# Performance work log

Hardware: AMD Instinct MI355X
Metric: run time of the kernel (lower is better)

Reference implementation:

```python
import jax, jax.numpy as jnp
import numpy as np

B, W, WIN_IN = 8, 2048, 1024
D, NH, DFF, L, KS = 512, 8, 2048, 4, 4
NGENES, G = 20000, 2048


def _ln(x, g, b, eps=1e-5):
    m = jnp.mean(x, -1, keepdims=True)
    v = jnp.var(x, -1, keepdims=True)
    return (x - m) * jax.lax.rsqrt(v + eps) * g + b


def _mha(q_in, kv_in, qkv_w, qkv_b, out_w, out_b, nh):
    d = q_in.shape[-1]
    hd = d // nh
    wq, wk, wv = qkv_w[:d], qkv_w[d:2 * d], qkv_w[2 * d:]
    bq, bk, bv = qkv_b[:d], qkv_b[d:2 * d], qkv_b[2 * d:]
    q = (q_in @ wq.T + bq).reshape(q_in.shape[0], q_in.shape[1], nh, hd)
    k = (kv_in @ wk.T + bk).reshape(kv_in.shape[0], kv_in.shape[1], nh, hd)
    v = (kv_in @ wv.T + bv).reshape(kv_in.shape[0], kv_in.shape[1], nh, hd)
    scores = jnp.einsum('bqhd,bkhd->bhqk', q, k) / jnp.sqrt(jnp.asarray(hd, q.dtype))
    a = jax.nn.softmax(scores, axis=-1)
    o = jnp.einsum('bhqk,bkhd->bqhd', a, v).reshape(q_in.shape[0], q_in.shape[1], d)
    return o @ out_w.T + out_b


def _posenc(S, d, dtype):
    pos = jnp.arange(S, dtype=jnp.float32)[:, None]
    div = jnp.exp(jnp.arange(0, d, 2, dtype=jnp.float32) * (-np.log(10000.0) / d))
    pe = jnp.zeros((S, d), jnp.float32)
    pe = pe.at[:, 0::2].set(jnp.sin(pos * div)).at[:, 1::2].set(jnp.cos(pos * div))
    return pe.astype(dtype)


def setup_inputs():
    key = jax.random.key(0)
    ks_ = jax.random.split(key, 12)

    def n(k, shape, s=0.02):
        return jax.random.normal(k, shape, jnp.float32) * s

    return dict(
        windows=jax.random.normal(ks_[0], (B, W, WIN_IN), jnp.float32),
        gene_ids=jax.random.randint(ks_[1], (G,), 0, NGENES),
        W_window=n(ks_[2], (D, WIN_IN)),
        enc_qkv_w=n(ks_[3], (L, 3 * D, D)),
        enc_qkv_b=jnp.zeros((L, 3 * D), jnp.float32),
        enc_out_w=n(ks_[4], (L, D, D)),
        enc_out_b=jnp.zeros((L, D), jnp.float32),
        enc_ln1_g=jnp.ones((L, D), jnp.float32),
        enc_ln1_b=jnp.zeros((L, D), jnp.float32),
        enc_ln2_g=jnp.ones((L, D), jnp.float32),
        enc_ln2_b=jnp.zeros((L, D), jnp.float32),
        enc_ff1_w=n(ks_[5], (L, DFF, D)),
        enc_ff1_b=jnp.zeros((L, DFF), jnp.float32),
        enc_ff2_w=n(ks_[6], (L, D, DFF)),
        enc_ff2_b=jnp.zeros((L, D), jnp.float32),
        gene_embed=n(ks_[7], (NGENES, D), 1.0),
        ca_qkv_w=n(ks_[8], (3 * D, D)),
        ca_qkv_b=jnp.zeros((3 * D,), jnp.float32),
        ca_out_w=n(ks_[9], (D, D)),
        ca_out_b=jnp.zeros((D,), jnp.float32),
        ro_ln_g=jnp.ones((D,), jnp.float32),
        ro_ln_b=jnp.zeros((D,), jnp.float32),
        ro_w=n(ks_[10], (1, D)),
        ro_b=jnp.zeros((1,), jnp.float32),
    )


def reference(windows, gene_ids, W_window, enc_qkv_w, enc_qkv_b, enc_out_w,
              enc_out_b, enc_ln1_g, enc_ln1_b, enc_ln2_g, enc_ln2_b,
              enc_ff1_w, enc_ff1_b, enc_ff2_w, enc_ff2_b, gene_embed,
              ca_qkv_w, ca_qkv_b, ca_out_w, ca_out_b, ro_ln_g, ro_ln_b,
              ro_w, ro_b):
    # proj_window (Linear, no bias; dropout inactive in eval)
    x = windows @ W_window.T                          # [B, W, D]
    Bn, Wn, _ = x.shape
    # AvgPool1d(kernel=stride=KS) along the window axis
    x = x.reshape(Bn, Wn // KS, KS, D).mean(axis=2)   # [B, S, D]
    S = x.shape[1]
    x = x + _posenc(S, D, x.dtype)[None]
    # pre-LN TransformerEncoder, relu FFN, no final norm
    for i in range(L):
        h = _ln(x, enc_ln1_g[i], enc_ln1_b[i])
        x = x + _mha(h, h, enc_qkv_w[i], enc_qkv_b[i], enc_out_w[i], enc_out_b[i], NH)
        h = _ln(x, enc_ln2_g[i], enc_ln2_b[i])
        x = x + (jax.nn.relu(h @ enc_ff1_w[i].T + enc_ff1_b[i]) @ enc_ff2_w[i].T + enc_ff2_b[i])
    # gene queries -> cross attention over encoded windows
    q = jnp.broadcast_to(gene_embed[gene_ids][None], (Bn, gene_ids.shape[0], D))
    z = _mha(q, x, ca_qkv_w, ca_qkv_b, ca_out_w, ca_out_b, NH)   # [B, G, D]
    pred = (_ln(z, ro_ln_g, ro_ln_b) @ ro_w.T + ro_b)[..., 0]    # [B, G]
    return pred, z
```

## Files before the change

kernel.cpp:

```cpp
#include <hip/hip_runtime.h>
#include <math.h>


typedef __attribute__((ext_vector_type(8))) short short8v;
typedef __attribute__((ext_vector_type(4))) float float4v;
typedef const __attribute__((address_space(1))) void* gas_t;
typedef __attribute__((address_space(3))) void* las_t;

__device__ inline unsigned short f2bf(float f) {
    unsigned int u = __builtin_bit_cast(unsigned int, f);
    return (unsigned short)((u + 0x7fffu + ((u >> 16) & 1u)) >> 16);
}

__device__ inline unsigned cvt_pk_bf16(float lo, float hi) {
    unsigned r;
    asm("v_cvt_pk_bf16_f32 %0, %1, %2" : "=v"(r) : "v"(lo), "v"(hi));
    return r;
}

__global__ __launch_bounds__(256) void cvt_all_k(
    const float* __restrict__ s0, const float* __restrict__ s1, const float* __restrict__ s2,
    const float* __restrict__ s3, const float* __restrict__ s4, const float* __restrict__ s5,
    const float* __restrict__ s6, unsigned short* __restrict__ dst)
{
    constexpr int c1 = 131072, c2 = 917504, c3 = 1179648, c4 = 2228224, c5 = 3276800, c6 = 3473408;
    int i = blockIdx.x * 256 + threadIdx.x;
    const float* s = s0; int base = 0;
    if (i >= c1) { s = s1; base = c1; }
    if (i >= c2) { s = s2; base = c2; }
    if (i >= c3) { s = s3; base = c3; }
    if (i >= c4) { s = s4; base = c4; }
    if (i >= c5) { s = s5; base = c5; }
    if (i >= c6) { s = s6; base = c6; }
    float4 v = ((const float4*)s)[i - base];
    ushort4 o;
    o.x = f2bf(v.x); o.y = f2bf(v.y); o.z = f2bf(v.z); o.w = f2bf(v.w);
    ((ushort4*)dst)[i] = o;
}

__global__ __launch_bounds__(256) void pool_windows_k(const float* __restrict__ win,
                                                      unsigned short* __restrict__ pw)
{
    int idx = blockIdx.x * 256 + threadIdx.x;
    int n = idx >> 8, c4 = (idx & 255) << 2;
    const float* base = win + (size_t)n * 4096 + c4;
    float4 a = *(const float4*)(base);
    float4 b2 = *(const float4*)(base + 1024);
    float4 c = *(const float4*)(base + 2048);
    float4 d = *(const float4*)(base + 3072);
    ushort4 r;
    r.x = f2bf((a.x + b2.x + c.x + d.x) * 0.25f);
    r.y = f2bf((a.y + b2.y + c.y + d.y) * 0.25f);
    r.z = f2bf((a.z + b2.z + c.z + d.z) * 0.25f);
    r.w = f2bf((a.w + b2.w + c.w + d.w) * 0.25f);
    ((ushort4*)pw)[idx] = r;
}

template<int BM, int BN, bool BIAS, bool BROW, bool RES, bool RELU, bool POSENC, bool O32, bool O16>
__global__ __launch_bounds__(256) void gemm_bf16_k(
    const unsigned short* __restrict__ A, const unsigned short* __restrict__ Bw,
    const float* __restrict__ bias, const float* __restrict__ Res,
    float* __restrict__ C32, unsigned short* __restrict__ C16,
    int M, int N, int K)
{
    constexpr int BK   = 64;
    constexpr int CPR  = BK / 8;
    constexpr int WR   = 2, WC = 2;
    constexpr int MSTEP = BM / WR;
    constexpr int NSTEP = BN / WC;
    constexpr int MFR  = MSTEP / 16;
    constexpr int NFR  = NSTEP / 16;
    constexpr int LPTA = BM * BK / 2048;
    constexpr int LPTB = BN * BK / 2048;
    constexpr int LPT  = LPTA + LPTB;
    __shared__ __align__(16) unsigned short As[3][BM * BK];
    __shared__ __align__(16) unsigned short Bs[3][BN * BK];
    const int tid = threadIdx.x;
    const int lane = tid & 63;
    const int m0 = blockIdx.x * BM, n0 = blockIdx.y * BN;
    const int wid = tid >> 6;
    const int wr = wid >> 1, wc = wid & 1;
    const int r = lane & 15, g = lane >> 4;

    const unsigned short* gA[LPTA];
    const unsigned short* gB[LPTB];
    #pragma unroll
    for (int j = 0; j < LPTA; ++j) {
        int c = tid + j * 256, row = c / CPR, cc = c % CPR;
        gA[j] = A + (size_t)(m0 + row) * K + ((cc ^ (row & (CPR - 1))) * 8);
    }
    #pragma unroll
    for (int j = 0; j < LPTB; ++j) {
        int c = tid + j * 256, row = c / CPR, cc = c % CPR;
        gB[j] = Bw + (size_t)(n0 + row) * K + ((cc ^ (row & (CPR - 1))) * 8);
    }

    auto stage = [&](int bi, int k0) {
        #pragma unroll
        for (int j = 0; j < LPTA; ++j)
            __builtin_amdgcn_global_load_lds((gas_t)(gA[j] + k0), (las_t)(&As[bi][(tid + j * 256) * 8]), 16, 0, 0);
        #pragma unroll
        for (int j = 0; j < LPTB; ++j)
            __builtin_amdgcn_global_load_lds((gas_t)(gB[j] + k0), (las_t)(&Bs[bi][(tid + j * 256) * 8]), 16, 0, 0);
    };

    float4v acc[MFR][NFR];
    float4v z4 = {0.f, 0.f, 0.f, 0.f};
    #pragma unroll
    for (int i = 0; i < MFR; ++i)
        #pragma unroll
        for (int j = 0; j < NFR; ++j) acc[i][j] = z4;

    const int S = K / BK;
    stage(0, 0);
    if (S > 1) stage(1, BK);
    for (int i = 0; i < S; ++i) {
        const int bi = i % 3;
        if (i + 2 < S) {
            stage((i + 2) % 3, (i + 2) * BK);
            asm volatile("s_waitcnt vmcnt(8)" ::: "memory");
        } else if (i + 1 < S) {
            asm volatile("s_waitcnt vmcnt(4)" ::: "memory");
        } else {
            asm volatile("s_waitcnt vmcnt(0)" ::: "memory");
        }
        __builtin_amdgcn_sched_barrier(0);
        __builtin_amdgcn_s_barrier();
        __builtin_amdgcn_sched_barrier(0);
        #pragma unroll
        for (int kk = 0; kk < BK / 32; ++kk) {
            const int cx = ((kk * 4 + g) ^ (r & (CPR - 1))) * 8;
            short8v a[MFR], b[NFR];
            #pragma unroll
            for (int mi = 0; mi < MFR; ++mi)
                a[mi] = *(const short8v*)&As[bi][(MSTEP * wr + 16 * mi + r) * BK + cx];
            #pragma unroll
            for (int ni = 0; ni < NFR; ++ni)
                b[ni] = *(const short8v*)&Bs[bi][(NSTEP * wc + 16 * ni + r) * BK + cx];
            #pragma unroll
            for (int mi = 0; mi < MFR; ++mi)
                #pragma unroll
                for (int ni = 0; ni < NFR; ++ni)
                    acc[mi][ni] = __builtin_amdgcn_mfma_f32_16x16x32_bf16(a[mi], b[ni], acc[mi][ni], 0, 0, 0);
        }
        __builtin_amdgcn_sched_barrier(0);
        __builtin_amdgcn_s_barrier();
        __builtin_amdgcn_sched_barrier(0);
    }

    #pragma unroll
    for (int mi = 0; mi < MFR; ++mi) {
        #pragma unroll
        for (int ni = 0; ni < NFR; ++ni) {
            const int row0 = m0 + MSTEP * wr + 16 * mi + g * 4;
            const int col  = n0 + NSTEP * wc + 16 * ni + r;
            float bv = (BIAS && !BROW) ? bias[col] : 0.f;
            float fr = 0.f;
            if (POSENC) fr = __expf((float)(col & ~1) * -0.01798894600f);
            #pragma unroll
            for (int q = 0; q < 4; ++q) {
                const int row = row0 + q;
                float v = acc[mi][ni][q] + bv;
                if (BIAS && BROW) v += bias[row];
                if (POSENC) {
                    float ang = (float)(row & 511) * fr;
                    v += (col & 1) ? __cosf(ang) : __sinf(ang);
                }
                if (RES) v += Res[(size_t)row * N + col];
                if (RELU) v = fmaxf(v, 0.0f);
                if (O32) C32[(size_t)row * N + col] = v;
                if (O16) C16[(size_t)row * N + col] = f2bf(v);
            }
        }
    }
}

template<bool SPLIT>
__global__ __launch_bounds__(256) void flashc_k(
    const unsigned short* __restrict__ Qp, long long q_bs, int q_rs,
    const unsigned short* __restrict__ Kp, long long k_bs, int k_rs,
    const unsigned short* __restrict__ Vtp, long long v_hs, long long v_bs, int v_rs,
    unsigned short* __restrict__ Op, long long o_bs, int o_rs,
    unsigned short* __restrict__ opart, float2* __restrict__ Ml,
    int nsplit, int nc)
{
    constexpr float C1 = 0.18033688011112042f;
    __shared__ __align__(16) unsigned short Kb[2][64 * 64];
    __shared__ __align__(16) unsigned short Vb[2][64 * 64];
    __shared__ __align__(16) unsigned short Ps[64 * 64];
    const int qt = blockIdx.x, h = blockIdx.y, z = blockIdx.z;
    const int b = z / nsplit, s = z - b * nsplit;
    const unsigned short* Q  = Qp  + (size_t)b * q_bs + (size_t)h * 64;
    const unsigned short* Kg = Kp  + (size_t)b * k_bs + (size_t)h * 64 + (size_t)(s * nc * 64) * k_rs;
    const unsigned short* Vg = Vtp + (size_t)h * v_hs + (size_t)b * v_bs + (size_t)(s * nc) * 64;
    const int q0 = qt * 64;
    const int tid = threadIdx.x, lane = tid & 63, w = tid >> 6;
    const int r = lane & 15, g = lane >> 4;
    const int sw8 = (r & 7) * 8;
    const int cA = (g * 8) ^ sw8;
    const int cB = ((g + 4) * 8) ^ sw8;
    const int prow = (16 * w + r) * 64;

    const unsigned short* qrow = Q + (size_t)(q0 + 16 * w + r) * q_rs + g * 8;
    short8v qf0 = *(const short8v*)(qrow);
    short8v qf1 = *(const short8v*)(qrow + 32);

    const int r0 = tid >> 3, cc = tid & 7;
    const int srcc = (cc ^ (r0 & 7)) * 8;
    auto stage = [&](int bi, int c) {
        const unsigned short* kc_ = Kg + (size_t)c * 64 * k_rs;
        const unsigned short* vc_ = Vg + (size_t)c * 64;
        __builtin_amdgcn_global_load_lds((gas_t)(kc_ + (size_t)r0 * k_rs + srcc),
                                         (las_t)(&Kb[bi][tid * 8]), 16, 0, 0);
        __builtin_amdgcn_global_load_lds((gas_t)(kc_ + (size_t)(r0 + 32) * k_rs + srcc),
                                         (las_t)(&Kb[bi][(tid + 256) * 8]), 16, 0, 0);
        __builtin_amdgcn_global_load_lds((gas_t)(vc_ + (size_t)r0 * v_rs + srcc),
                                         (las_t)(&Vb[bi][tid * 8]), 16, 0, 0);
        __builtin_amdgcn_global_load_lds((gas_t)(vc_ + (size_t)(r0 + 32) * v_rs + srcc),
                                         (las_t)(&Vb[bi][(tid + 256) * 8]), 16, 0, 0);
    };

    float4v acc_o[4];
    float4v z4 = {0.f, 0.f, 0.f, 0.f};
    #pragma unroll
    for (int dt = 0; dt < 4; ++dt) acc_o[dt] = z4;
    float m_own = -INFINITY, l_own = 0.f;

    stage(0, 0);
    __syncthreads();
    int buf = 0;

    for (int c = 0; c < nc; ++c) {
        if (c + 1 < nc) stage(buf ^ 1, c + 1);
        const unsigned short* KL = Kb[buf];
        const unsigned short* VL = Vb[buf];

        __builtin_amdgcn_s_setprio(1);
        float4v accs[4];
        #pragma unroll
        for (int t = 0; t < 4; ++t) {
            accs[t] = z4;
            const unsigned short* krow = KL + (16 * t + r) * 64;
            short8v kf0 = *(const short8v*)(krow + cA);
            short8v kf1 = *(const short8v*)(krow + cB);
            accs[t] = __builtin_amdgcn_mfma_f32_16x16x32_bf16(kf0, qf0, accs[t], 0, 0, 0);
            accs[t] = __builtin_amdgcn_mfma_f32_16x16x32_bf16(kf1, qf1, accs[t], 0, 0, 0);
        }
        __builtin_amdgcn_s_setprio(0);

        float m0_ = fmaxf(fmaxf(accs[0][0], accs[0][1]), fmaxf(accs[0][2], accs[0][3]));
        float m1_ = fmaxf(fmaxf(accs[1][0], accs[1][1]), fmaxf(accs[1][2], accs[1][3]));
        float m2_ = fmaxf(fmaxf(accs[2][0], accs[2][1]), fmaxf(accs[2][2], accs[2][3]));
        float m3_ = fmaxf(fmaxf(accs[3][0], accs[3][1]), fmaxf(accs[3][2], accs[3][3]));
        float sm = fmaxf(fmaxf(m0_, m1_), fmaxf(m2_, m3_));
        sm = fmaxf(sm, __shfl_xor(sm, 16));
        sm = fmaxf(sm, __shfl_xor(sm, 32));

        if (__any(sm > m_own + 64.f)) {
            float mn = fmaxf(m_own, sm);
            float alpha = __builtin_amdgcn_exp2f((m_own - mn) * C1);
            m_own = mn;
            float a0_ = __shfl(alpha, g * 4 + 0);
            float a1_ = __shfl(alpha, g * 4 + 1);
            float a2_ = __shfl(alpha, g * 4 + 2);
            float a3_ = __shfl(alpha, g * 4 + 3);
            #pragma unroll
            for (int dt = 0; dt < 4; ++dt) {
                acc_o[dt][0] *= a0_; acc_o[dt][1] *= a1_;
                acc_o[dt][2] *= a2_; acc_o[dt][3] *= a3_;
            }
            l_own *= alpha;
        }

        const float m2c = m_own * C1;
        float p[4][4];
        float rsum = 0.f;
        #pragma unroll
        for (int t = 0; t < 4; ++t)
            #pragma unroll
            for (int j = 0; j < 4; ++j) {
                float pv = __builtin_amdgcn_exp2f(__builtin_fmaf(accs[t][j], C1, -m2c));
                p[t][j] = pv; rsum += pv;
            }
        rsum += __shfl_xor(rsum, 16);
        rsum += __shfl_xor(rsum, 32);
        l_own += rsum;

        #pragma unroll
        for (int t = 0; t < 4; ++t) {
            uint2 uu;
            uu.x = cvt_pk_bf16(p[t][0], p[t][1]);
            uu.y = cvt_pk_bf16(p[t][2], p[t][3]);
            int pc = (((2 * t + (g >> 1)) * 8) ^ sw8) + (g & 1) * 4;
            *(uint2*)&Ps[prow + pc] = uu;
        }

        __builtin_amdgcn_s_setprio(1);
        short8v pf0 = *(const short8v*)&Ps[prow + cA];
        short8v pf1 = *(const short8v*)&Ps[prow + cB];
        #pragma unroll
        for (int dt = 0; dt < 4; ++dt) {
            const unsigned short* vrow = VL + (16 * dt + r) * 64;
            short8v vf0 = *(const short8v*)(vrow + cA);
            short8v vf1 = *(const short8v*)(vrow + cB);
            acc_o[dt] = __builtin_amdgcn_mfma_f32_16x16x32_bf16(pf0, vf0, acc_o[dt], 0, 0, 0);
            acc_o[dt] = __builtin_amdgcn_mfma_f32_16x16x32_bf16(pf1, vf1, acc_o[dt], 0, 0, 0);
        }
        __builtin_amdgcn_s_setprio(0);

        __syncthreads();
        buf ^= 1;
    }

    float il0 = 1.f / __shfl(l_own, g * 4 + 0);
    float il1 = 1.f / __shfl(l_own, g * 4 + 1);
    float il2 = 1.f / __shfl(l_own, g * 4 + 2);
    float il3 = 1.f / __shfl(l_own, g * 4 + 3);
    if (SPLIT) {
        unsigned short* Ob = opart + ((size_t)(s * 4096 + b * 512)) * 512 + h * 64;
        #pragma unroll
        for (int dt = 0; dt < 4; ++dt) {
            Ob[(size_t)(q0 + 16 * w + g * 4 + 0) * 512 + 16 * dt + r] = f2bf(acc_o[dt][0] * il0);
            Ob[(size_t)(q0 + 16 * w + g * 4 + 1) * 512 + 16 * dt + r] = f2bf(acc_o[dt][1] * il1);
            Ob[(size_t)(q0 + 16 * w + g * 4 + 2) * 512 + 16 * dt + r] = f2bf(acc_o[dt][2] * il2);
            Ob[(size_t)(q0 + 16 * w + g * 4 + 3) * 512 + 16 * dt + r] = f2bf(acc_o[dt][3] * il3);
        }
        if (g == 0)
            Ml[((size_t)(s * 8 + b) * 8 + h) * 512 + q0 + 16 * w + r] = make_float2(m_own, l_own);
    } else {
        unsigned short* O = Op + (size_t)b * o_bs + (size_t)h * 64;
        #pragma unroll
        for (int dt = 0; dt < 4; ++dt) {
            O[(size_t)(q0 + 16 * w + g * 4 + 0) * o_rs + 16 * dt + r] = f2bf(acc_o[dt][0] * il0);
            O[(size_t)(q0 + 16 * w + g * 4 + 1) * o_rs + 16 * dt + r] = f2bf(acc_o[dt][1] * il1);
            O[(size_t)(q0 + 16 * w + g * 4 + 2) * o_rs + 16 * dt + r] = f2bf(acc_o[dt][2] * il2);
            O[(size_t)(q0 + 16 * w + g * 4 + 3) * o_rs + 16 * dt + r] = f2bf(acc_o[dt][3] * il3);
        }
    }
}

template<int NS>
__global__ __launch_bounds__(256) void combine_k(const unsigned short* __restrict__ opart,
                                                 const float2* __restrict__ Ml,
                                                 unsigned short* __restrict__ Oo)
{
    constexpr float C1 = 0.18033688011112042f;
    const int row = blockIdx.x;
    const int b = row >> 9, srow = row & 511;
    const int tid = threadIdx.x;
    const int h = tid >> 5, t = tid & 31;
    float2 ml[NS];
    float m = -INFINITY;
    #pragma unroll
    for (int s = 0; s < NS; ++s) {
        ml[s] = Ml[((size_t)(s * 8 + b) * 8 + h) * 512 + srow];
        m = fmaxf(m, ml[s].x);
    }
    float wgt[NS];
    float wsum = 0.f;
    #pragma unroll
    for (int s = 0; s < NS; ++s) {
        wgt[s] = __builtin_amdgcn_exp2f((ml[s].x - m) * C1) * ml[s].y;
        wsum += wgt[s];
    }
    float inv = 1.f / wsum;
    const int col = h * 64 + t * 2;
    float acc0 = 0.f, acc1 = 0.f;
    #pragma unroll
    for (int s = 0; s < NS; ++s) {
        unsigned u = *(const unsigned*)&opart[((size_t)s * 4096 + row) * 512 + col];
        acc0 += wgt[s] * __builtin_bit_cast(float, (u & 0xffffu) << 16);
        acc1 += wgt[s] * __builtin_bit_cast(float, (u >> 16) << 16);
    }
    *(unsigned*)&Oo[(size_t)row * 512 + col] = cvt_pk_bf16(acc0 * inv, acc1 * inv);
}

__global__ __launch_bounds__(64) void ln_k(const float* __restrict__ X, unsigned short* __restrict__ Y,
                                           const float* __restrict__ g, const float* __restrict__ bt)
{
    int row = blockIdx.x, lane = threadIdx.x;
    const float* x = X + (size_t)row * 512;
    int c0 = lane * 4, c1 = 256 + lane * 4;
    float4 a0 = *(const float4*)&x[c0];
    float4 a1 = *(const float4*)&x[c1];
    float s  = a0.x + a0.y + a0.z + a0.w + a1.x + a1.y + a1.z + a1.w;
    float ss = a0.x * a0.x + a0.y * a0.y + a0.z * a0.z + a0.w * a0.w
             + a1.x * a1.x + a1.y * a1.y + a1.z * a1.z + a1.w * a1.w;
    #pragma unroll
    for (int off = 1; off < 64; off <<= 1) { s += __shfl_xor(s, off); ss += __shfl_xor(ss, off); }
    float mean = s * (1.f / 512.f);
    float var  = ss * (1.f / 512.f) - mean * mean;
    float rs = rsqrtf(var + 1e-5f);
    float4 g0 = *(const float4*)&g[c0], g1 = *(const float4*)&g[c1];
    float4 b0 = *(const float4*)&bt[c0], b1 = *(const float4*)&bt[c1];
    unsigned short* y = Y + (size_t)row * 512;
    ushort4 o0, o1;
    o0.x = f2bf((a0.x - mean) * rs * g0.x + b0.x);  o0.y = f2bf((a0.y - mean) * rs * g0.y + b0.y);
    o0.z = f2bf((a0.z - mean) * rs * g0.z + b0.z);  o0.w = f2bf((a0.w - mean) * rs * g0.w + b0.w);
    o1.x = f2bf((a1.x - mean) * rs * g1.x + b1.x);  o1.y = f2bf((a1.y - mean) * rs * g1.y + b1.y);
    o1.z = f2bf((a1.z - mean) * rs * g1.z + b1.z);  o1.w = f2bf((a1.w - mean) * rs * g1.w + b1.w);
    *(ushort4*)&y[c0] = o0;
    *(ushort4*)&y[c1] = o1;
}

__global__ __launch_bounds__(128) void gather_k(const float* __restrict__ ge, const int* __restrict__ ids,
                                                unsigned short* __restrict__ out)
{
    int gi = blockIdx.x, t = threadIdx.x;
    int id = ids[gi];
    float4 v = *(const float4*)&ge[(size_t)id * 512 + t * 4];
    ushort4 o;
    o.x = f2bf(v.x); o.y = f2bf(v.y); o.z = f2bf(v.z); o.w = f2bf(v.w);
    *(ushort4*)&out[(size_t)gi * 512 + t * 4] = o;
}

__global__ __launch_bounds__(64) void readout_k(const float* __restrict__ Z,
                                                const float* __restrict__ g, const float* __restrict__ bt,
                                                const float* __restrict__ rw, const float* __restrict__ rb,
                                                float* __restrict__ pred)
{
    int row = blockIdx.x, lane = threadIdx.x;
    const float* zr = Z + (size_t)row * 512;
    int c0 = lane * 4, c1 = 256 + lane * 4;
    float4 a0 = *(const float4*)&zr[c0];
    float4 a1 = *(const float4*)&zr[c1];
    float s  = a0.x + a0.y + a0.z + a0.w + a1.x + a1.y + a1.z + a1.w;
    float ss = a0.x * a0.x + a0.y * a0.y + a0.z * a0.z + a0.w * a0.w
             + a1.x * a1.x + a1.y * a1.y + a1.z * a1.z + a1.w * a1.w;
    #pragma unroll
    for (int off = 1; off < 64; off <<= 1) { s += __shfl_xor(s, off); ss += __shfl_xor(ss, off); }
    float mean = s * (1.f / 512.f);
    float var  = ss * (1.f / 512.f) - mean * mean;
    float rs = rsqrtf(var + 1e-5f);
    float4 g0 = *(const float4*)&g[c0], g1 = *(const float4*)&g[c1];
    float4 b0 = *(const float4*)&bt[c0], b1 = *(const float4*)&bt[c1];
    float4 w0 = *(const float4*)&rw[c0], w1 = *(const float4*)&rw[c1];
    float acc = 0.f;
    acc += ((a0.x - mean) * rs * g0.x + b0.x) * w0.x;
    acc += ((a0.y - mean) * rs * g0.y + b0.y) * w0.y;
    acc += ((a0.z - mean) * rs * g0.z + b0.z) * w0.z;
    acc += ((a0.w - mean) * rs * g0.w + b0.w) * w0.w;
    acc += ((a1.x - mean) * rs * g1.x + b1.x) * w1.x;
    acc += ((a1.y - mean) * rs * g1.y + b1.y) * w1.y;
    acc += ((a1.z - mean) * rs * g1.z + b1.z) * w1.z;
    acc += ((a1.w - mean) * rs * g1.w + b1.w) * w1.w;
    #pragma unroll
    for (int off = 1; off < 64; off <<= 1) acc += __shfl_xor(acc, off);
    if (lane == 0) pred[row] = acc + rb[0];
}

extern "C" void kernel_launch(void* const* d_in, const int* in_sizes, int n_in,
                              void* d_out, int out_size, void* d_ws, size_t ws_size,
                              hipStream_t stream)
{
    (void)in_sizes; (void)n_in; (void)out_size; (void)ws_size;
    const float* windows    = (const float*)d_in[0];
    const int*   gene_ids   = (const int*)  d_in[1];
    const float* W_window   = (const float*)d_in[2];
    const float* enc_qkv_w  = (const float*)d_in[3];
    const float* enc_qkv_b  = (const float*)d_in[4];
    const float* enc_out_w  = (const float*)d_in[5];
    const float* enc_out_b  = (const float*)d_in[6];
    const float* enc_ln1_g  = (const float*)d_in[7];
    const float* enc_ln1_b  = (const float*)d_in[8];
    const float* enc_ln2_g  = (const float*)d_in[9];
    const float* enc_ln2_b  = (const float*)d_in[10];
    const float* enc_ff1_w  = (const float*)d_in[11];
    const float* enc_ff1_b  = (const float*)d_in[12];
    const float* enc_ff2_w  = (const float*)d_in[13];
    const float* enc_ff2_b  = (const float*)d_in[14];
    const float* gene_embed = (const float*)d_in[15];
    const float* ca_qkv_w   = (const float*)d_in[16];
    const float* ca_qkv_b   = (const float*)d_in[17];
    const float* ca_out_w   = (const float*)d_in[18];
    const float* ca_out_b   = (const float*)d_in[19];
    const float* ro_ln_g    = (const float*)d_in[20];
    const float* ro_ln_b    = (const float*)d_in[21];
    const float* ro_w       = (const float*)d_in[22];
    const float* ro_b       = (const float*)d_in[23];

    float* pred = (float*)d_out;
    float* z    = pred + (size_t)8 * 2048;

    char* wp = (char*)d_ws;
    float* x = (float*)wp;                       wp += (size_t)4096 * 512 * 4;
    unsigned short* x16   = (unsigned short*)wp; wp += (size_t)4096 * 512 * 2;
    unsigned short* h16   = (unsigned short*)wp; wp += (size_t)4096 * 512 * 2;
    unsigned short* qkv16 = (unsigned short*)wp; wp += (size_t)4096 * 1536 * 2;
    unsigned short* ao16  = (unsigned short*)wp; wp += (size_t)4096 * 512 * 2;
    unsigned short* big16 = (unsigned short*)wp; wp += (size_t)16384 * 512 * 2;
    unsigned short* vt16  = (unsigned short*)wp; wp += (size_t)512 * 4096 * 2;
    unsigned short* wall16 = (unsigned short*)wp;
    unsigned short* wW16     = wall16;
    unsigned short* wqkv16   = wW16     + (size_t)512 * 1024;
    unsigned short* wout16   = wqkv16   + (size_t)4 * 1536 * 512;
    unsigned short* wff116   = wout16   + (size_t)4 * 512 * 512;
    unsigned short* wff216   = wff116   + (size_t)4 * 2048 * 512;
    unsigned short* wcaqkv16 = wff216   + (size_t)4 * 512 * 2048;
    unsigned short* wcaout16 = wcaqkv16 + (size_t)1536 * 512;
    unsigned short* pw16    = big16;
    unsigned short* ff116   = big16;
    unsigned short* oc16    = big16;
    unsigned short* opart16 = big16;
    float2* mlbuf = (float2*)(qkv16 + (size_t)4096 * 1024);
    unsigned short* ge16  = qkv16;
    unsigned short* qg16  = qkv16 + (size_t)2048 * 512;
    unsigned short* kc16  = qkv16 + (size_t)2 * 2048 * 512;

    cvt_all_k<<<13824, 256, 0, stream>>>(W_window, enc_qkv_w, enc_out_w, enc_ff1_w,
                                         enc_ff2_w, ca_qkv_w, ca_out_w, wall16);

    pool_windows_k<<<4096, 256, 0, stream>>>(windows, pw16);
    gemm_bf16_k<64, 64, false, false, false, false, true, true, false><<<dim3(64, 8), 256, 0, stream>>>(
        pw16, wW16, nullptr, nullptr, x, nullptr, 4096, 512, 1024);

    for (int l = 0; l < 4; ++l) {
        const unsigned short* wl = wqkv16 + (size_t)l * 1536 * 512;
        ln_k<<<4096, 64, 0, stream>>>(x, h16, enc_ln1_g + l * 512, enc_ln1_b + l * 512);
        gemm_bf16_k<64, 64, true, false, false, false, false, false, true><<<dim3(64, 16), 256, 0, stream>>>(
            h16, wl, enc_qkv_b + l * 1536, nullptr, nullptr, qkv16, 4096, 1024, 512);
        gemm_bf16_k<64, 64, true, true, false, false, false, false, true><<<dim3(8, 64), 256, 0, stream>>>(
            wl + (size_t)1024 * 512, h16, enc_qkv_b + l * 1536 + 1024, nullptr,
            nullptr, vt16, 512, 4096, 512);
        flashc_k<true><<<dim3(8, 8, 32), 256, 0, stream>>>(
            qkv16, (long long)512 * 1024, 1024,
            qkv16 + 512, (long long)512 * 1024, 1024,
            vt16, (long long)64 * 4096, 512LL, 4096,
            nullptr, 0LL, 0,
            opart16, mlbuf, 4, 2);
        combine_k<4><<<4096, 256, 0, stream>>>(opart16, mlbuf, ao16);
        gemm_bf16_k<64, 64, true, false, true, false, false, true, false><<<dim3(64, 8), 256, 0, stream>>>(
            ao16, wout16 + (size_t)l * 512 * 512, enc_out_b + l * 512, x, x, nullptr, 4096, 512, 512);
        ln_k<<<4096, 64, 0, stream>>>(x, h16, enc_ln2_g + l * 512, enc_ln2_b + l * 512);
        gemm_bf16_k<64, 64, true, false, false, true, false, false, true><<<dim3(64, 32), 256, 0, stream>>>(
            h16, wff116 + (size_t)l * 2048 * 512, enc_ff1_b + l * 2048, nullptr,
            nullptr, ff116, 4096, 2048, 512);
        if (l == 3)
            gemm_bf16_k<64, 64, true, false, true, false, false, true, true><<<dim3(64, 8), 256, 0, stream>>>(
                ff116, wff216 + (size_t)l * 512 * 2048, enc_ff2_b + l * 512, x, x, x16, 4096, 512, 2048);
        else
            gemm_bf16_k<64, 64, true, false, true, false, false, true, false><<<dim3(64, 8), 256, 0, stream>>>(
                ff116, wff216 + (size_t)l * 512 * 2048, enc_ff2_b + l * 512, x, x, nullptr, 4096, 512, 2048);
    }

    gather_k<<<2048, 128, 0, stream>>>(gene_embed, gene_ids, ge16);
    gemm_bf16_k<64, 64, true, false, false, false, false, false, true><<<dim3(32, 8), 256, 0, stream>>>(
        ge16, wcaqkv16, ca_qkv_b, nullptr, nullptr, qg16, 2048, 512, 512);
    gemm_bf16_k<64, 64, true, false, false, false, false, false, true><<<dim3(64, 8), 256, 0, stream>>>(
        x16, wcaqkv16 + (size_t)512 * 512, ca_qkv_b + 512, nullptr, nullptr, kc16, 4096, 512, 512);
    gemm_bf16_k<64, 64, true, true, false, false, false, false, true><<<dim3(8, 64), 256, 0, stream>>>(
        wcaqkv16 + (size_t)1024 * 512, x16, ca_qkv_b + 1024, nullptr, nullptr, vt16, 512, 4096, 512);
    flashc_k<false><<<dim3(32, 8, 8), 256, 0, stream>>>(
        qg16, 0LL, 512,
        kc16, (long long)512 * 512, 512,
        vt16, (long long)64 * 4096, 512LL, 4096,
        oc16, (long long)2048 * 512, 512,
        nullptr, nullptr, 1, 8);
    gemm_bf16_k<64, 64, true, false, false, false, false, true, false><<<dim3(256, 8), 256, 0, stream>>>(
        oc16, wcaout16, ca_out_b, nullptr, z, nullptr, 16384, 512, 512);

    readout_k<<<16384, 64, 0, stream>>>(z, ro_ln_g, ro_ln_b, ro_w, ro_b, pred);
}
```

Baseline: 560.0 us.

## Split cross-attention KV over two partitions and switch GEMM to double buffering

```diff
diff --git a/kernel.cpp b/kernel.cpp
--- a/kernel.cpp
+++ b/kernel.cpp
@@ -63,9 +63,10 @@
     float* __restrict__ C32, unsigned short* __restrict__ C16,
     int M, int N, int K)
 {
-    constexpr int BK   = 64;
+    constexpr int BK   = (BM == 128) ? 32 : 64;
     constexpr int CPR  = BK / 8;
-    constexpr int WR   = 2, WC = 2;
+    constexpr int WR   = (BM == 64 && BN == 128) ? 1 : 2;
+    constexpr int WC   = 4 / WR;
     constexpr int MSTEP = BM / WR;
     constexpr int NSTEP = BN / WC;
     constexpr int MFR  = MSTEP / 16;
@@ -73,13 +74,13 @@
     constexpr int LPTA = BM * BK / 2048;
     constexpr int LPTB = BN * BK / 2048;
     constexpr int LPT  = LPTA + LPTB;
-    __shared__ __align__(16) unsigned short As[3][BM * BK];
-    __shared__ __align__(16) unsigned short Bs[3][BN * BK];
+    __shared__ __align__(16) unsigned short As[2][BM * BK];
+    __shared__ __align__(16) unsigned short Bs[2][BN * BK];
     const int tid = threadIdx.x;
     const int lane = tid & 63;
     const int m0 = blockIdx.x * BM, n0 = blockIdx.y * BN;
     const int wid = tid >> 6;
-    const int wr = wid >> 1, wc = wid & 1;
+    const int wr = wid / WC, wc = wid % WC;
     const int r = lane & 15, g = lane >> 4;
 
     const unsigned short* gA[LPTA];
@@ -111,16 +112,13 @@
         #pragma unroll
         for (int j = 0; j < NFR; ++j) acc[i][j] = z4;
 
-    const int S = K / BK;
     stage(0, 0);
-    if (S > 1) stage(1, BK);
-    for (int i = 0; i < S; ++i) {
-        const int bi = i % 3;
-        if (i + 2 < S) {
-            stage((i + 2) % 3, (i + 2) * BK);
-            asm volatile("s_waitcnt vmcnt(8)" ::: "memory");
-        } else if (i + 1 < S) {
-            asm volatile("s_waitcnt vmcnt(4)" ::: "memory");
+    int buf = 0;
+    for (int k0 = 0; k0 < K; k0 += BK) {
+        if (k0 + BK < K) {
+            stage(buf ^ 1, k0 + BK);
+            if constexpr (LPT == 4) asm volatile("s_waitcnt vmcnt(4)" ::: "memory");
+            else                    asm volatile("s_waitcnt vmcnt(6)" ::: "memory");
         } else {
             asm volatile("s_waitcnt vmcnt(0)" ::: "memory");
         }
@@ -133,10 +131,10 @@
             short8v a[MFR], b[NFR];
             #pragma unroll
             for (int mi = 0; mi < MFR; ++mi)
-                a[mi] = *(const short8v*)&As[bi][(MSTEP * wr + 16 * mi + r) * BK + cx];
+                a[mi] = *(const short8v*)&As[buf][(MSTEP * wr + 16 * mi + r) * BK + cx];
             #pragma unroll
             for (int ni = 0; ni < NFR; ++ni)
-                b[ni] = *(const short8v*)&Bs[bi][(NSTEP * wc + 16 * ni + r) * BK + cx];
+                b[ni] = *(const short8v*)&Bs[buf][(NSTEP * wc + 16 * ni + r) * BK + cx];
             #pragma unroll
             for (int mi = 0; mi < MFR; ++mi)
                 #pragma unroll
@@ -145,7 +143,7 @@
         }
         __builtin_amdgcn_sched_barrier(0);
         __builtin_amdgcn_s_barrier();
-        __builtin_amdgcn_sched_barrier(0);
+        buf ^= 1;
     }
 
     #pragma unroll
@@ -181,8 +179,8 @@
     const unsigned short* __restrict__ Kp, long long k_bs, int k_rs,
     const unsigned short* __restrict__ Vtp, long long v_hs, long long v_bs, int v_rs,
     unsigned short* __restrict__ Op, long long o_bs, int o_rs,
-    unsigned short* __restrict__ opart, float2* __restrict__ Ml,
-    int nsplit, int nc)
+    unsigned short* __restrict__ opart, long long part_stride, int q_rows,
+    float2* __restrict__ Ml, int nsplit, int nc)
 {
     constexpr float C1 = 0.18033688011112042f;
     __shared__ __align__(16) unsigned short Kb[2][64 * 64];
@@ -317,7 +315,8 @@
     float il2 = 1.f / __shfl(l_own, g * 4 + 2);
     float il3 = 1.f / __shfl(l_own, g * 4 + 3);
     if (SPLIT) {
-        unsigned short* Ob = opart + ((size_t)(s * 4096 + b * 512)) * 512 + h * 64;
+        unsigned short* Ob = opart + (size_t)s * part_stride
+                           + ((size_t)(b * q_rows)) * 512 + h * 64;
         #pragma unroll
         for (int dt = 0; dt < 4; ++dt) {
             Ob[(size_t)(q0 + 16 * w + g * 4 + 0) * 512 + 16 * dt + r] = f2bf(acc_o[dt][0] * il0);
@@ -326,7 +325,7 @@
             Ob[(size_t)(q0 + 16 * w + g * 4 + 3) * 512 + 16 * dt + r] = f2bf(acc_o[dt][3] * il3);
         }
         if (g == 0)
-            Ml[((size_t)(s * 8 + b) * 8 + h) * 512 + q0 + 16 * w + r] = make_float2(m_own, l_own);
+            Ml[((size_t)(s * 8 + b) * 8 + h) * q_rows + q0 + 16 * w + r] = make_float2(m_own, l_own);
     } else {
         unsigned short* O = Op + (size_t)b * o_bs + (size_t)h * 64;
         #pragma unroll
@@ -339,21 +338,22 @@
     }
 }
 
-template<int NS>
+template<int NS, int QROWS>
 __global__ __launch_bounds__(256) void combine_k(const unsigned short* __restrict__ opart,
+                                                 long long part_stride,
                                                  const float2* __restrict__ Ml,
                                                  unsigned short* __restrict__ Oo)
 {
     constexpr float C1 = 0.18033688011112042f;
     const int row = blockIdx.x;
-    const int b = row >> 9, srow = row & 511;
+    const int b = row / QROWS, srow = row % QROWS;
     const int tid = threadIdx.x;
     const int h = tid >> 5, t = tid & 31;
     float2 ml[NS];
     float m = -INFINITY;
     #pragma unroll
     for (int s = 0; s < NS; ++s) {
-        ml[s] = Ml[((size_t)(s * 8 + b) * 8 + h) * 512 + srow];
+        ml[s] = Ml[((size_t)(s * 8 + b) * 8 + h) * QROWS + srow];
         m = fmaxf(m, ml[s].x);
     }
     float wgt[NS];
@@ -368,7 +368,7 @@
     float acc0 = 0.f, acc1 = 0.f;
     #pragma unroll
     for (int s = 0; s < NS; ++s) {
-        unsigned u = *(const unsigned*)&opart[((size_t)s * 4096 + row) * 512 + col];
+        unsigned u = *(const unsigned*)&opart[(size_t)s * part_stride + (size_t)row * 512 + col];
         acc0 += wgt[s] * __builtin_bit_cast(float, (u & 0xffffu) << 16);
         acc1 += wgt[s] * __builtin_bit_cast(float, (u >> 16) << 16);
     }
@@ -482,7 +482,8 @@
     float* pred = (float*)d_out;
     float* z    = pred + (size_t)8 * 2048;
 
-    char* wp = (char*)d_ws;
+    char* wsb = (char*)d_ws;
+    char* wp = wsb;
     float* x = (float*)wp;                       wp += (size_t)4096 * 512 * 4;
     unsigned short* x16   = (unsigned short*)wp; wp += (size_t)4096 * 512 * 2;
     unsigned short* h16   = (unsigned short*)wp; wp += (size_t)4096 * 512 * 2;
@@ -506,6 +507,8 @@
     unsigned short* ge16  = qkv16;
     unsigned short* qg16  = qkv16 + (size_t)2048 * 512;
     unsigned short* kc16  = qkv16 + (size_t)2 * 2048 * 512;
+    unsigned short* copart = (unsigned short*)wsb;
+    const long long cstride = (long long)16 * 1024 * 1024;
 
     cvt_all_k<<<13824, 256, 0, stream>>>(W_window, enc_qkv_w, enc_out_w, enc_ff1_w,
                                          enc_ff2_w, ca_qkv_w, ca_out_w, wall16);
@@ -527,8 +530,8 @@
             qkv16 + 512, (long long)512 * 1024, 1024,
             vt16, (long long)64 * 4096, 512LL, 4096,
             nullptr, 0LL, 0,
-            opart16, mlbuf, 4, 2);
-        combine_k<4><<<4096, 256, 0, stream>>>(opart16, mlbuf, ao16);
+            opart16, (long long)4096 * 512, 512, mlbuf, 4, 2);
+        combine_k<4, 512><<<4096, 256, 0, stream>>>(opart16, (long long)4096 * 512, mlbuf, ao16);
         gemm_bf16_k<64, 64, true, false, true, false, false, true, false><<<dim3(64, 8), 256, 0, stream>>>(
             ao16, wout16 + (size_t)l * 512 * 512, enc_out_b + l * 512, x, x, nullptr, 4096, 512, 512);
         ln_k<<<4096, 64, 0, stream>>>(x, h16, enc_ln2_g + l * 512, enc_ln2_b + l * 512);
@@ -550,12 +553,13 @@
         x16, wcaqkv16 + (size_t)512 * 512, ca_qkv_b + 512, nullptr, nullptr, kc16, 4096, 512, 512);
     gemm_bf16_k<64, 64, true, true, false, false, false, false, true><<<dim3(8, 64), 256, 0, stream>>>(
         wcaqkv16 + (size_t)1024 * 512, x16, ca_qkv_b + 1024, nullptr, nullptr, vt16, 512, 4096, 512);
-    flashc_k<false><<<dim3(32, 8, 8), 256, 0, stream>>>(
+    flashc_k<true><<<dim3(32, 8, 16), 256, 0, stream>>>(
         qg16, 0LL, 512,
         kc16, (long long)512 * 512, 512,
         vt16, (long long)64 * 4096, 512LL, 4096,
-        oc16, (long long)2048 * 512, 512,
-        nullptr, nullptr, 1, 8);
+        nullptr, 0LL, 0,
+        copart, cstride, 2048, mlbuf, 2, 4);
+    combine_k<2, 2048><<<16384, 256, 0, stream>>>(copart, cstride, mlbuf, oc16);
     gemm_bf16_k<64, 64, true, false, false, false, false, true, false><<<dim3(256, 8), 256, 0, stream>>>(
         oc16, wcaout16, ca_out_b, nullptr, z, nullptr, 16384, 512, 512);
 
```

After: 546.6 us. 2.4% less time.
